# Kernel optimization log

Hardware: AMD Instinct MI355X
Metric: run time of the kernel (lower is better)

The kernel has to match this reference:

```python
import math
import jax, jax.numpy as jnp
import numpy as np

# Dims (match init_kwargs)
B, S, HID = 2, 2048, 2048
H, KVH, D = 16, 8, 128
ATTN_H = 8                      # softmax heads (head_split_dict)
TN_H = H - ATTN_H               # linear (tnorm) heads
N_REP = H // KVH                # GQA repeat factor
FIRST_TOKENS, LAST_TOKENS = 64, 512  # global prefix + band width for custom mask
EPS = 1e-6
ROPE_BASE = 1e6
SCALE = 1.0 / math.sqrt(D)


def _rope_tables(seq_len):
    inv_freq = 1.0 / (ROPE_BASE ** (jnp.arange(0, D, 2, dtype=jnp.float32) / D))
    t = jnp.arange(seq_len, dtype=jnp.float32)
    freqs = jnp.outer(t, inv_freq)                 # [S, D/2]
    emb = jnp.concatenate([freqs, freqs], axis=-1)  # [S, D]
    return jnp.cos(emb), jnp.sin(emb)


def _rotate_half(x):
    x1, x2 = jnp.split(x, 2, axis=-1)
    return jnp.concatenate([-x2, x1], axis=-1)


def _apply_rope(x, cos, sin):
    # x: [B, h, S, D], cos/sin: [S, D]
    return x * cos[None, None] + _rotate_half(x) * sin[None, None]


def _rms_norm(x):
    # SimpleRMSNorm: computed in fp32, no learned weight
    xf = x.astype(jnp.float32)
    out = xf * jax.lax.rsqrt(jnp.mean(xf * xf, axis=-1, keepdims=True) + EPS)
    return out.astype(x.dtype)


def setup_inputs() -> dict:
    key = jax.random.key(0)
    ks = jax.random.split(key, 6)
    sc = 0.02
    perm_np = np.array([3, 7, 0, 12, 9, 15, 1, 5, 2, 4, 6, 8, 10, 11, 13, 14], np.int32)
    inv_np = np.zeros(H, np.int32)
    inv_np[perm_np] = np.arange(H, dtype=np.int32)
    return {
        'hidden_states': jax.random.normal(ks[0], (B, S, HID), jnp.float32),
        'q_w': jax.random.normal(ks[1], (HID, HID), jnp.float32) * sc,
        'q_b': jnp.zeros((HID,), jnp.float32),
        'k_w': jax.random.normal(ks[2], (KVH * D, HID), jnp.float32) * sc,
        'k_b': jnp.zeros((KVH * D,), jnp.float32),
        'v_w': jax.random.normal(ks[3], (KVH * D, HID), jnp.float32) * sc,
        'v_b': jnp.zeros((KVH * D,), jnp.float32),
        'o_w': jax.random.normal(ks[4], (HID, HID), jnp.float32) * sc,
        'head_policy': jnp.array([1, 0, 1, 0, 1, 0, 1, 0], dtype=bool),
        'perm': jnp.asarray(perm_np),
        'inv_perm': jnp.asarray(inv_np),
    }


def _custom_mask(head_policy):
    # create_custom_causal_mask: banded causal + global prefix for heads with
    # policy==False; plain causal for heads with policy==True. Additive mask.
    qi = jnp.arange(S)[:, None]
    ki = jnp.arange(S)[None, :]
    causal = ki <= qi
    band = causal & ((qi - ki) < LAST_TOKENS)
    band = band | ((ki < FIRST_TOKENS) & (qi >= FIRST_TOKENS))
    neg = jnp.finfo(jnp.float32).min
    orig = jnp.where(causal, 0.0, neg)
    new = jnp.where(band, 0.0, neg)
    return jnp.where(head_policy[:, None, None], orig, new), causal  # [ATTN_H,S,S]


def reference(hidden_states, q_w, q_b, k_w, k_b, v_w, v_b, o_w,
              head_policy, perm, inv_perm):
    dt = hidden_states.dtype
    q = hidden_states @ q_w.T + q_b           # [B,S,HID]
    k = hidden_states @ k_w.T + k_b           # [B,S,KVH*D]
    v = hidden_states @ v_w.T + v_b

    # head permutation on q, then split softmax vs tnorm heads
    q = q.reshape(B, S, H, D)[:, :, perm, :]
    q = jnp.transpose(q, (0, 2, 1, 3))        # [B,H,S,D]
    kh = jnp.transpose(k.reshape(B, S, KVH, D), (0, 2, 1, 3))  # [B,KVH,S,D]
    vh = jnp.transpose(v.reshape(B, S, KVH, D), (0, 2, 1, 3))

    cos, sin = _rope_tables(S)
    q = _apply_rope(q, cos, sin)              # rope on all q heads (both branches)
    kh = _apply_rope(kh, cos, sin)

    # repeat_kv (GQA) then head permutation
    k_all = jnp.repeat(kh, N_REP, axis=1)[:, perm]  # [B,H,S,D]
    v_all = jnp.repeat(vh, N_REP, axis=1)[:, perm]

    # ---- softmax branch (first ATTN_H heads), custom banded/global mask ----
    mask, causal = _custom_mask(head_policy)
    logits = jnp.einsum('bhqd,bhkd->bhqk', q[:, :ATTN_H], k_all[:, :ATTN_H]) * SCALE
    logits = logits + mask[None]
    probs = jax.nn.softmax(logits.astype(jnp.float32), axis=-1).astype(dt)
    out_sm = jnp.einsum('bhqk,bhkd->bhqd', probs, v_all[:, :ATTN_H])
    out_sm = jnp.transpose(out_sm, (0, 2, 1, 3)).reshape(B, S, ATTN_H * D)

    # ---- linear (tnorm) branch (remaining heads): masked qk^T @ v + RMSNorm ----
    w = jnp.einsum('bhqd,bhkd->bhqk', q[:, ATTN_H:], k_all[:, ATTN_H:]) * SCALE
    w = jnp.where(causal[None, None], w, jnp.zeros((), dt))
    out_tn = jnp.einsum('bhqk,bhkd->bhqd', w, v_all[:, ATTN_H:])
    out_tn = jnp.transpose(out_tn, (0, 2, 1, 3)).reshape(B, S, TN_H * D)
    out_tn = _rms_norm(out_tn)

    # concat heads, undo permutation, output projection
    out = jnp.concatenate([out_sm, out_tn], axis=-1)
    out = out.reshape(B, S, H, D)[:, :, inv_perm, :].reshape(B, S, HID)
    return out @ o_w.T
```

## Files before the change

kernel.cpp:

```cpp
#include <hip/hip_runtime.h>
#include <hip/hip_bf16.h>
#include <stdint.h>

#define AS1 __attribute__((address_space(1)))
#define AS3 __attribute__((address_space(3)))

typedef __bf16 bf16x8 __attribute__((ext_vector_type(8)));
typedef unsigned short u16x8 __attribute__((ext_vector_type(8)));
typedef float f32x4 __attribute__((ext_vector_type(4)));

static __device__ __forceinline__ unsigned short f2bf(float f) {
  unsigned u = __float_as_uint(f);
  u += 0x7fffu + ((u >> 16) & 1u);
  return (unsigned short)(u >> 16);
}
static __device__ __forceinline__ float bf2f(unsigned short h) {
  return __uint_as_float(((unsigned)h) << 16);
}
static __device__ __forceinline__ bf16x8 ld_frag(const unsigned short* p) {
  union { u16x8 u; bf16x8 b; } c;
  c.u = *(const u16x8*)p;
  return c.b;
}
static __device__ __forceinline__ void gload16(const void* g, void* l) {
  __builtin_amdgcn_global_load_lds((AS1 const void*)g, (AS3 void*)l, 16, 0, 0);
}
#define MFMA(a, b, c) __builtin_amdgcn_mfma_f32_16x16x32_bf16(a, b, c, 0, 0, 0)
#define BAR asm volatile("s_barrier" ::: "memory")
#define VM4 asm volatile("s_waitcnt vmcnt(4)" ::: "memory")

__global__ __launch_bounds__(256)
void cvt_all(const float* __restrict__ hs, const float* __restrict__ qw,
             const float* __restrict__ kw, const float* __restrict__ vw,
             unsigned short* __restrict__ hbf, unsigned short* __restrict__ wqkv) {
  long i = (long)blockIdx.x * 256 + threadIdx.x;
  const float* src; unsigned short* dst; long off;
  if (i < 2097152)      { src = hs; dst = hbf;            off = i; }
  else if (i < 3145728) { src = qw; dst = wqkv;           off = i - 2097152; }
  else if (i < 3670016) { src = kw; dst = wqkv + 4194304; off = i - 3145728; }
  else                  { src = vw; dst = wqkv + 6291456; off = i - 3670016; }
  float4 f = *(const float4*)&src[off * 4];
  ushort4 u;
  u.x = f2bf(f.x); u.y = f2bf(f.y); u.z = f2bf(f.z); u.w = f2bf(f.w);
  *(ushort4*)&dst[off * 4] = u;
}

__global__ __launch_bounds__(256)
void cvt4(const float* __restrict__ in, unsigned short* __restrict__ out, long n) {
  long i = ((long)blockIdx.x * 256 + threadIdx.x) * 4;
  if (i >= n) return;
  float4 f = *(const float4*)&in[i];
  ushort4 u;
  u.x = f2bf(f.x); u.y = f2bf(f.y); u.z = f2bf(f.z); u.w = f2bf(f.w);
  *(ushort4*)&out[i] = u;
}

__global__ __launch_bounds__(256)
void rope_apply(unsigned short* __restrict__ qh, unsigned short* __restrict__ kh) {
  long i = (long)blockIdx.x * 256 + threadIdx.x;
  const long QT = (long)2 * 16 * 2048 * 64;
  unsigned short* p; long rem; float outsc;
  if (i < QT) { p = qh; rem = i; outsc = 0.08838834764831845f; }
  else        { p = kh; rem = i - QT; outsc = 1.0f; }
  int j = (int)(rem & 63);
  long row = rem >> 6;
  int s = (int)(row & 2047);
  unsigned short* x = p + row * 128;
  float inv = exp2f(-0.31143075889569023f * (float)j);
  float f = (float)s * inv;
  float sn, c;
  sincosf(f, &sn, &c);
  float x1 = bf2f(x[j]), x2 = bf2f(x[j + 64]);
  x[j]      = f2bf((x1 * c - x2 * sn) * outsc);
  x[j + 64] = f2bf((x2 * c + x1 * sn) * outsc);
}

__global__ __launch_bounds__(512, 2)
void gemm256_qkv(const unsigned short* __restrict__ A,
                 const unsigned short* __restrict__ Bw,
                 const float* __restrict__ qb, const float* __restrict__ kb,
                 const float* __restrict__ vb,
                 unsigned short* __restrict__ qh, unsigned short* __restrict__ kh,
                 unsigned short* __restrict__ vT) {
  constexpr int K = 2048, NT = K / 64, NIT = NT / 2;
  __shared__ alignas(16) unsigned short LDS[65536];
  const int id = blockIdx.x;
  const int lg = (id & 7) * 32 + (id >> 3);
  const int bm = lg >> 4, bn = lg & 15;
  const int tid = threadIdx.x;
  const int wid = tid >> 6, lane = tid & 63;
  const int wr = wid >> 2, wc = wid & 3;
  const int l15 = lane & 15, lhi = lane >> 4;
  const int rsw = (l15 & 7) << 3;
  const int srow0 = wid * 8 + (lane >> 3);
  const int scol = ((lane & 7) ^ (lane >> 3)) * 8;
  const unsigned short* Ag = A + (long)(bm * 256) * K;
  const unsigned short* Bg = Bw + (long)(bn * 256) * K;
  unsigned short* Al = LDS;
  unsigned short* Bl = LDS + 32768;

#define STG(gb, lb, p, h, t) do {                                              \
    int tc = (t) < NT ? (t) : NT - 1;                                          \
    gload16((gb) + (long)((h) * 128 + srow0) * K + tc * 64 + scol,             \
            (lb) + (p) * 16384 + (h) * 8192 + wid * 512);                      \
    gload16((gb) + (long)((h) * 128 + 64 + srow0) * K + tc * 64 + scol,        \
            (lb) + (p) * 16384 + (h) * 8192 + 4096 + wid * 512);               \
  } while (0)

#define LDA(p, mh) do {                                                        \
    _Pragma("unroll") for (int m4 = 0; m4 < 4; ++m4)                           \
    _Pragma("unroll") for (int kk = 0; kk < 2; ++kk)                           \
      afr[m4][kk] = ld_frag(&Al[(p) * 16384 +                                  \
          (wr * 128 + (mh) * 64 + m4 * 16 + l15) * 64 +                        \
          ((kk * 32 + lhi * 8) ^ rsw)]);                                       \
  } while (0)

#define LDB(p, nh) do {                                                        \
    _Pragma("unroll") for (int n2 = 0; n2 < 2; ++n2)                           \
    _Pragma("unroll") for (int kk = 0; kk < 2; ++kk)                           \
      bfr[nh][n2][kk] = ld_frag(&Bl[(p) * 16384 +                              \
          (wc * 64 + (nh) * 32 + n2 * 16 + l15) * 64 +                         \
          ((kk * 32 + lhi * 8) ^ rsw)]);                                       \
  } while (0)

#define QUAD(mh, nh) do {                                                      \
    __builtin_amdgcn_s_setprio(1);                                             \
    _Pragma("unroll") for (int m4 = 0; m4 < 4; ++m4)                           \
    _Pragma("unroll") for (int n2 = 0; n2 < 2; ++n2)                           \
    _Pragma("unroll") for (int kk = 0; kk < 2; ++kk)                           \
      acc[(mh) * 4 + m4][(nh) * 2 + n2] =                                      \
          MFMA(afr[m4][kk], bfr[nh][n2][kk], acc[(mh) * 4 + m4][(nh) * 2 + n2]);\
    __builtin_amdgcn_s_setprio(0);                                             \
  } while (0)

  f32x4 acc[8][4] = {};
  bf16x8 afr[4][2], bfr[2][2][2];

  STG(Bg, Bl, 0, 0, 0); STG(Bg, Bl, 0, 1, 0);
  STG(Ag, Al, 0, 0, 0); STG(Ag, Al, 0, 1, 0);
  STG(Bg, Bl, 1, 0, 1); STG(Bg, Bl, 1, 1, 1);
  VM4; BAR;

  for (int it = 0; it < NIT; ++it) {
    const int T = 2 * it;
    LDA(0, 0); LDB(0, 0); STG(Ag, Al, 1, 0, T + 1);
    BAR; QUAD(0, 0); BAR;
    LDB(0, 1);            STG(Ag, Al, 1, 1, T + 1);
    BAR; QUAD(0, 1); BAR;
    LDA(0, 1);            STG(Bg, Bl, 0, 0, T + 2);
    BAR; QUAD(1, 0); BAR;
                          STG(Bg, Bl, 0, 1, T + 2);
    VM4; BAR; QUAD(1, 1); BAR;
    LDA(1, 0); LDB(1, 0); STG(Ag, Al, 0, 0, T + 2);
    BAR; QUAD(0, 0); BAR;
    LDB(1, 1);            STG(Ag, Al, 0, 1, T + 2);
    BAR; QUAD(0, 1); BAR;
    LDA(1, 1);            STG(Bg, Bl, 1, 0, T + 3);
    BAR; QUAD(1, 0); BAR;
                          STG(Bg, Bl, 1, 1, T + 3);
    VM4; BAR; QUAD(1, 1); BAR;
  }

  const int r0 = bm * 256 + wr * 128, c0 = bn * 256 + wc * 64;
#pragma unroll
  for (int m = 0; m < 8; ++m) {
#pragma unroll
    for (int n = 0; n < 4; ++n) {
#pragma unroll
      for (int j = 0; j < 4; ++j) {
        int row = r0 + m * 16 + lhi * 4 + j;
        int col = c0 + n * 16 + l15;
        float v = acc[m][n][j];
        int b = row >> 11, s = row & 2047;
        if (col < 2048) {
          v += qb[col];
          qh[((long)(b * 16 + (col >> 7)) * 2048 + s) * 128 + (col & 127)] = f2bf(v);
        } else if (col < 3072) {
          int c = col - 2048; v += kb[c];
          kh[((long)(b * 8 + (c >> 7)) * 2048 + s) * 128 + (c & 127)] = f2bf(v);
        } else {
          int c = col - 3072; v += vb[c];
          vT[((long)(b * 8 + (c >> 7)) * 128 + (c & 127)) * 2048 + s] = f2bf(v);
        }
      }
    }
  }
#undef STG
#undef LDA
#undef LDB
#undef QUAD
}

__global__ __launch_bounds__(256, 2)
void gemm_bt(const unsigned short* __restrict__ A,
             const unsigned short* __restrict__ Bw,
             int K, int N, float* __restrict__ Cout) {
  __shared__ alignas(16) unsigned short As[128 * 64];
  __shared__ alignas(16) unsigned short Bs[128 * 64];
  const int bm = blockIdx.x, bn = blockIdx.y;
  const int tid = threadIdx.x;
  const int w = tid >> 6, l = tid & 63;
  const int wm = w >> 1, wn = w & 1;
  const int l15 = l & 15, lhi = l >> 4;
  f32x4 acc[4][4] = {};
  const unsigned short* aptr = A + ((long)(bm * 128 + w * 8 + (l >> 3))) * K + (l & 7) * 8;
  const unsigned short* bptr = Bw + ((long)(bn * 128 + w * 8 + (l >> 3))) * K + (l & 7) * 8;
  unsigned short* asb = &As[w * 8 * 64];
  unsigned short* bsb = &Bs[w * 8 * 64];
  for (int k0 = 0; k0 < K; k0 += 64) {
#pragma unroll
    for (int i = 0; i < 4; ++i) {
      gload16(aptr + (long)i * 32 * K, asb + i * 2048);
      gload16(bptr + (long)i * 32 * K, bsb + i * 2048);
    }
    aptr += 64; bptr += 64;
    __syncthreads();
#pragma unroll
    for (int kk = 0; kk < 2; ++kk) {
      bf16x8 af[4], bfr[4];
#pragma unroll
      for (int m = 0; m < 4; ++m)
        af[m] = ld_frag(&As[(wm * 64 + m * 16 + l15) * 64 + kk * 32 + lhi * 8]);
#pragma unroll
      for (int n = 0; n < 4; ++n)
        bfr[n] = ld_frag(&Bs[(wn * 64 + n * 16 + l15) * 64 + kk * 32 + lhi * 8]);
#pragma unroll
      for (int m = 0; m < 4; ++m)
#pragma unroll
        for (int n = 0; n < 4; ++n)
          acc[m][n] = MFMA(af[m], bfr[n], acc[m][n]);
    }
    __syncthreads();
  }
#pragma unroll
  for (int m = 0; m < 4; ++m)
#pragma unroll
    for (int n = 0; n < 4; ++n)
#pragma unroll
      for (int j = 0; j < 4; ++j) {
        int row = bm * 128 + wm * 64 + m * 16 + lhi * 4 + j;
        int col = bn * 128 + wn * 64 + n * 16 + l15;
        Cout[(long)row * N + col] = acc[m][n][j];
      }
}

__global__ __launch_bounds__(256, 4)
void attn_all(const unsigned short* __restrict__ qheads,
              const unsigned short* __restrict__ kheads,
              const unsigned short* __restrict__ vT,
              unsigned short* __restrict__ aout,
              unsigned short* __restrict__ tnb,
              unsigned short* __restrict__ pao0, unsigned short* __restrict__ pao1,
              float* __restrict__ pl0, float* __restrict__ pl1,
              const int* __restrict__ perm) {
  __shared__ alignas(16) unsigned short Ks[64 * 128];
  __shared__ alignas(16) unsigned short Vs[128 * 64];
  __shared__ alignas(16) unsigned short Ps[4][16 * 64];
  const int bx = 47 - blockIdx.x;
  const int hy = blockIdx.y;
  const int b = blockIdx.z;
  const bool sm = hy < 8;
  const bool banded = sm && ((hy & 1) != 0);
  int t, kst, ket;
  bool partial = false, slice1 = false;
  if (banded) {
    if (bx >= 32) return;
    t = bx; kst = 0; ket = t;
  } else if (bx < 16) {
    t = bx; kst = 0; ket = t;
  } else if (bx < 32) {
    t = bx; int h = (t + 2) >> 1; kst = 0; ket = h - 1; partial = true;
  } else {
    t = bx - 16; int h = (t + 2) >> 1; kst = h; ket = t; partial = true; slice1 = true;
  }
  const int q0 = t * 64;
  const int qhd = perm[hy];
  const int kvh = qhd >> 1;
  const int tid = threadIdx.x, w = tid >> 6, l = tid & 63, l15 = l & 15, lhi = l >> 4;
  const unsigned short* Qg = qheads + ((long)(b * 16 + qhd) * 2048 + q0) * 128;
  const unsigned short* Kg = kheads + (long)(b * 8 + kvh) * 2048 * 128;
  const unsigned short* Vg = vT + (long)(b * 8 + kvh) * 128 * 2048;
  bf16x8 qf[4];
#pragma unroll
  for (int c = 0; c < 4; ++c)
    qf[c] = ld_frag(Qg + (w * 16 + l15) * 128 + c * 32 + lhi * 8);
  f32x4 ao[8] = {};
  float lsum[4] = {0.f, 0.f, 0.f, 0.f};
  const int krow = w * 4 + (l >> 4);
  const long kgoff = (long)krow * 128 + (((l & 15) * 8) ^ ((krow & 7) << 3));
  unsigned short* kdst = &Ks[w * 512];
  const int vrow = w * 8 + (l >> 3);
  const long vgoff = (long)vrow * 2048 + (((l & 7) * 8) ^ ((vrow & 7) << 3));
  unsigned short* vdst = &Vs[w * 512];
  const int rsw15 = (l15 & 7) << 3;

  for (int k0 = kst * 64; k0 <= ket * 64; k0 += 64) {
    if (banded && k0 >= 64 && q0 - k0 >= 575) continue;
    __syncthreads();
#pragma unroll
    for (int p = 0; p < 4; ++p)
      gload16(Kg + (long)(k0 + p * 16) * 128 + kgoff, kdst + p * 2048);
#pragma unroll
    for (int p = 0; p < 4; ++p)
      gload16(Vg + (long)p * 32 * 2048 + k0 + vgoff, vdst + p * 2048);
    __syncthreads();
    f32x4 sacc[4] = {};
    __builtin_amdgcn_s_setprio(1);
#pragma unroll
    for (int c = 0; c < 4; ++c) {
#pragma unroll
      for (int ks = 0; ks < 4; ++ks) {
        bf16x8 kf = ld_frag(&Ks[(ks * 16 + l15) * 128 + ((c * 32 + lhi * 8) ^ rsw15)]);
        sacc[ks] = MFMA(qf[c], kf, sacc[ks]);
      }
    }
    __builtin_amdgcn_s_setprio(0);
    const int qrb = q0 + w * 16 + lhi * 4;
#pragma unroll
    for (int j = 0; j < 4; ++j) {
      const int q = qrb + j;
      const int prow = lhi * 4 + j;
      const int psw = (prow & 7) << 3;
#pragma unroll
      for (int ks = 0; ks < 4; ++ks) {
        int k = k0 + ks * 16 + l15;
        bool ok = (k <= q) && (!banded || k < 64 || (q - k) < 512);
        float p;
        if (sm) { p = ok ? __expf(sacc[ks][j]) : 0.f; lsum[j] += p; }
        else    { p = ok ? sacc[ks][j] : 0.f; }
        Ps[w][prow * 64 + ((ks * 16 + l15) ^ psw)] = f2bf(p);
      }
    }
    bf16x8 pa0 = ld_frag(&Ps[w][l15 * 64 + ((lhi * 8) ^ rsw15)]);
    bf16x8 pa1 = ld_frag(&Ps[w][l15 * 64 + ((32 + lhi * 8) ^ rsw15)]);
    __builtin_amdgcn_s_setprio(1);
#pragma unroll
    for (int n = 0; n < 8; ++n) {
      bf16x8 vf0 = ld_frag(&Vs[(n * 16 + l15) * 64 + ((lhi * 8) ^ rsw15)]);
      bf16x8 vf1 = ld_frag(&Vs[(n * 16 + l15) * 64 + ((32 + lhi * 8) ^ rsw15)]);
      ao[n] = MFMA(pa0, vf0, ao[n]);
      ao[n] = MFMA(pa1, vf1, ao[n]);
    }
    __builtin_amdgcn_s_setprio(0);
  }

  if (partial) {
    const int hc = sm ? (hy >> 1) : (hy - 4);
    const long rbase = (long)(b * 12 + hc) * 1024 + (q0 - 1024);
    unsigned short* pb = (slice1 ? pao1 : pao0) + rbase * 128;
    float* plb = (slice1 ? pl1 : pl0) + rbase;
#pragma unroll
    for (int j = 0; j < 4; ++j) {
      const int r = w * 16 + lhi * 4 + j;
      if (sm) {
        float s = lsum[j];
#pragma unroll
        for (int d = 1; d < 16; d <<= 1) s += __shfl_xor(s, d);
        if (l15 == 0) plb[r] = s;
      }
#pragma unroll
      for (int n = 0; n < 8; ++n)
        pb[(long)r * 128 + n * 16 + l15] = f2bf(ao[n][j]);
    }
  } else if (sm) {
#pragma unroll
    for (int j = 0; j < 4; ++j) {
      float s = lsum[j];
#pragma unroll
      for (int d = 1; d < 16; d <<= 1) s += __shfl_xor(s, d);
      float inv = 1.0f / s;
      int q = q0 + w * 16 + lhi * 4 + j;
      unsigned short* o = aout + ((long)b * 2048 + q) * 2048 + qhd * 128;
#pragma unroll
      for (int n = 0; n < 8; ++n) o[n * 16 + l15] = f2bf(ao[n][j] * inv);
    }
  } else {
    const int hidx = hy - 8;
#pragma unroll
    for (int j = 0; j < 4; ++j) {
      int q = q0 + w * 16 + lhi * 4 + j;
      unsigned short* o = tnb + ((long)b * 2048 + q) * 1024 + hidx * 128;
#pragma unroll
      for (int n = 0; n < 8; ++n) o[n * 16 + l15] = f2bf(ao[n][j]);
    }
  }
}

__global__ __launch_bounds__(256)
void combine(const unsigned short* __restrict__ pao0,
             const unsigned short* __restrict__ pao1,
             const float* __restrict__ pl0, const float* __restrict__ pl1,
             unsigned short* __restrict__ aout, unsigned short* __restrict__ tnb,
             const int* __restrict__ perm) {
  long i = (long)blockIdx.x * 256 + threadIdx.x;
  long row = i >> 7;
  int col = (int)(i & 127);
  int b = (int)(row / 12288);
  int rem = (int)(row - (long)b * 12288);
  int hc = rem >> 10;
  int q = 1024 + (rem & 1023);
  float a = bf2f(pao0[i]) + bf2f(pao1[i]);
  if (hc < 4) {
    int qhd = perm[hc * 2];
    float lv = pl0[row] + pl1[row];
    aout[((long)b * 2048 + q) * 2048 + qhd * 128 + col] = f2bf(a / lv);
  } else {
    tnb[((long)b * 2048 + q) * 1024 + (hc - 4) * 128 + col] = f2bf(a);
  }
}

__global__ __launch_bounds__(256)
void rms_scatter(const unsigned short* __restrict__ tnb,
                 unsigned short* __restrict__ aout,
                 const int* __restrict__ perm) {
  __shared__ float wsum[4];
  int row = blockIdx.x, tid = threadIdx.x;
  const unsigned short* x = tnb + (long)row * 1024;
  ushort4 u = *(const ushort4*)&x[tid * 4];
  float v0 = bf2f(u.x), v1 = bf2f(u.y), v2 = bf2f(u.z), v3 = bf2f(u.w);
  float ss = v0 * v0 + v1 * v1 + v2 * v2 + v3 * v3;
#pragma unroll
  for (int d = 1; d < 64; d <<= 1) ss += __shfl_xor(ss, d);
  if ((tid & 63) == 0) wsum[tid >> 6] = ss;
  __syncthreads();
  float tot = wsum[0] + wsum[1] + wsum[2] + wsum[3];
  float r = rsqrtf(tot * (1.0f / 1024.0f) + 1e-6f);
  int slot = perm[8 + (tid >> 5)];
  unsigned short* o = aout + (long)row * 2048 + slot * 128 + ((tid * 4) & 127);
  o[0] = f2bf(v0 * r); o[1] = f2bf(v1 * r); o[2] = f2bf(v2 * r); o[3] = f2bf(v3 * r);
}

extern "C" void kernel_launch(void* const* d_in, const int* in_sizes, int n_in,
                              void* d_out, int out_size, void* d_ws, size_t ws_size,
                              hipStream_t stream) {
  const float* hs  = (const float*)d_in[0];
  const float* q_w = (const float*)d_in[1];
  const float* q_b = (const float*)d_in[2];
  const float* k_w = (const float*)d_in[3];
  const float* k_b = (const float*)d_in[4];
  const float* v_w = (const float*)d_in[5];
  const float* v_b = (const float*)d_in[6];
  const float* o_w = (const float*)d_in[7];
  const int* perm  = (const int*)d_in[9];

  char* ws = (char*)d_ws;
  unsigned short* hbf  = (unsigned short*)(ws + 0);
  unsigned short* wqkv = (unsigned short*)(ws + 16777216);
  unsigned short* kh   = (unsigned short*)(ws + 33554432);
  unsigned short* vT   = (unsigned short*)(ws + 41943040);
  char* dob = (char*)d_out;
  unsigned short* qh   = (unsigned short*)dob;
  unsigned short* pao0 = (unsigned short*)(dob + 16777216);
  unsigned short* pao1 = (unsigned short*)(dob + 23068672);
  float* pl0           = (float*)(dob + 29360128);
  float* pl1           = (float*)(dob + 29458432);
  unsigned short* aout = hbf;
  unsigned short* tnb  = wqkv;
  unsigned short* owb  = kh;
  float* outF = (float*)d_out;

  cvt_all<<<16384, 256, 0, stream>>>(hs, q_w, k_w, v_w, hbf, wqkv);
  gemm256_qkv<<<256, 512, 0, stream>>>(hbf, wqkv, q_b, k_b, v_b, qh, kh, vT);
  rope_apply<<<24576, 256, 0, stream>>>(qh, kh);
  attn_all<<<dim3(48, 16, 2), 256, 0, stream>>>(qh, kh, vT, aout, tnb,
                                                pao0, pao1, pl0, pl1, perm);
  combine<<<12288, 256, 0, stream>>>(pao0, pao1, pl0, pl1, aout, tnb, perm);
  cvt4<<<4096, 256, 0, stream>>>(o_w, owb, 4194304);
  rms_scatter<<<4096, 256, 0, stream>>>(tnb, aout, perm);
  gemm_bt<<<dim3(32, 16), 256, 0, stream>>>(aout, owb, 2048, 2048, outF);
}
```

Baseline: 276.5 us.

## Split PV matmul across warps by output columns instead of query rows

The P·V step now shares the probability tiles of all four warps through LDS. Each warp computes 32 of the 128 output columns for all 64 query rows, rather than all columns for its own 16 rows. This cuts the V-fragment LDS reads per warp from 16 to 4, and the extra work is reading the other warps' P tiles. It adds a block-wide barrier per key tile and an LDS buffer for the row sums, and the epilogue changes to match the new ownership of the output.

```diff
diff --git a/kernel.cpp b/kernel.cpp
--- a/kernel.cpp
+++ b/kernel.cpp
@@ -256,6 +256,7 @@
   __shared__ alignas(16) unsigned short Ks[64 * 128];
   __shared__ alignas(16) unsigned short Vs[128 * 64];
   __shared__ alignas(16) unsigned short Ps[4][16 * 64];
+  __shared__ float Ls[64];
   const int bx = 47 - blockIdx.x;
   const int hy = blockIdx.y;
   const int b = blockIdx.z;
@@ -284,7 +285,7 @@
 #pragma unroll
   for (int c = 0; c < 4; ++c)
     qf[c] = ld_frag(Qg + (w * 16 + l15) * 128 + c * 32 + lhi * 8);
-  f32x4 ao[8] = {};
+  f32x4 ao[2][4] = {};
   float lsum[4] = {0.f, 0.f, 0.f, 0.f};
   const int krow = w * 4 + (l >> 4);
   const long kgoff = (long)krow * 128 + (((l & 15) * 8) ^ ((krow & 7) << 3));
@@ -331,58 +332,72 @@
         Ps[w][prow * 64 + ((ks * 16 + l15) ^ psw)] = f2bf(p);
       }
     }
-    bf16x8 pa0 = ld_frag(&Ps[w][l15 * 64 + ((lhi * 8) ^ rsw15)]);
-    bf16x8 pa1 = ld_frag(&Ps[w][l15 * 64 + ((32 + lhi * 8) ^ rsw15)]);
+    __syncthreads();
     __builtin_amdgcn_s_setprio(1);
-#pragma unroll
-    for (int n = 0; n < 8; ++n) {
-      bf16x8 vf0 = ld_frag(&Vs[(n * 16 + l15) * 64 + ((lhi * 8) ^ rsw15)]);
-      bf16x8 vf1 = ld_frag(&Vs[(n * 16 + l15) * 64 + ((32 + lhi * 8) ^ rsw15)]);
-      ao[n] = MFMA(pa0, vf0, ao[n]);
-      ao[n] = MFMA(pa1, vf1, ao[n]);
+    bf16x8 vf0a = ld_frag(&Vs[((w * 2) * 16 + l15) * 64 + ((lhi * 8) ^ rsw15)]);
+    bf16x8 vf1a = ld_frag(&Vs[((w * 2) * 16 + l15) * 64 + ((32 + lhi * 8) ^ rsw15)]);
+    bf16x8 vf0b = ld_frag(&Vs[((w * 2 + 1) * 16 + l15) * 64 + ((lhi * 8) ^ rsw15)]);
+    bf16x8 vf1b = ld_frag(&Vs[((w * 2 + 1) * 16 + l15) * 64 + ((32 + lhi * 8) ^ rsw15)]);
+#pragma unroll
+    for (int wc = 0; wc < 4; ++wc) {
+      bf16x8 pa0 = ld_frag(&Ps[wc][l15 * 64 + ((lhi * 8) ^ rsw15)]);
+      bf16x8 pa1 = ld_frag(&Ps[wc][l15 * 64 + ((32 + lhi * 8) ^ rsw15)]);
+      ao[0][wc] = MFMA(pa0, vf0a, ao[0][wc]);
+      ao[0][wc] = MFMA(pa1, vf1a, ao[0][wc]);
+      ao[1][wc] = MFMA(pa0, vf0b, ao[1][wc]);
+      ao[1][wc] = MFMA(pa1, vf1b, ao[1][wc]);
     }
     __builtin_amdgcn_s_setprio(0);
   }
+
+#pragma unroll
+  for (int j = 0; j < 4; ++j) {
+    float s = lsum[j];
+#pragma unroll
+    for (int d = 1; d < 16; d <<= 1) s += __shfl_xor(s, d);
+    if (l15 == 0) Ls[w * 16 + lhi * 4 + j] = s;
+  }
+  __syncthreads();
 
   if (partial) {
     const int hc = sm ? (hy >> 1) : (hy - 4);
     const long rbase = (long)(b * 12 + hc) * 1024 + (q0 - 1024);
     unsigned short* pb = (slice1 ? pao1 : pao0) + rbase * 128;
     float* plb = (slice1 ? pl1 : pl0) + rbase;
-#pragma unroll
-    for (int j = 0; j < 4; ++j) {
-      const int r = w * 16 + lhi * 4 + j;
-      if (sm) {
-        float s = lsum[j];
-#pragma unroll
-        for (int d = 1; d < 16; d <<= 1) s += __shfl_xor(s, d);
-        if (l15 == 0) plb[r] = s;
-      }
-#pragma unroll
-      for (int n = 0; n < 8; ++n)
-        pb[(long)r * 128 + n * 16 + l15] = f2bf(ao[n][j]);
-    }
+    if (sm && tid < 64) plb[tid] = Ls[tid];
+#pragma unroll
+    for (int wc = 0; wc < 4; ++wc)
+#pragma unroll
+      for (int j = 0; j < 4; ++j) {
+        int r = wc * 16 + lhi * 4 + j;
+#pragma unroll
+        for (int n2 = 0; n2 < 2; ++n2)
+          pb[(long)r * 128 + (w * 2 + n2) * 16 + l15] = f2bf(ao[n2][wc][j]);
+      }
   } else if (sm) {
 #pragma unroll
-    for (int j = 0; j < 4; ++j) {
-      float s = lsum[j];
-#pragma unroll
-      for (int d = 1; d < 16; d <<= 1) s += __shfl_xor(s, d);
-      float inv = 1.0f / s;
-      int q = q0 + w * 16 + lhi * 4 + j;
-      unsigned short* o = aout + ((long)b * 2048 + q) * 2048 + qhd * 128;
-#pragma unroll
-      for (int n = 0; n < 8; ++n) o[n * 16 + l15] = f2bf(ao[n][j] * inv);
-    }
+    for (int wc = 0; wc < 4; ++wc)
+#pragma unroll
+      for (int j = 0; j < 4; ++j) {
+        int r = wc * 16 + lhi * 4 + j;
+        float inv = 1.0f / Ls[r];
+        unsigned short* o = aout + ((long)b * 2048 + q0 + r) * 2048 + qhd * 128;
+#pragma unroll
+        for (int n2 = 0; n2 < 2; ++n2)
+          o[(w * 2 + n2) * 16 + l15] = f2bf(ao[n2][wc][j] * inv);
+      }
   } else {
     const int hidx = hy - 8;
 #pragma unroll
-    for (int j = 0; j < 4; ++j) {
-      int q = q0 + w * 16 + lhi * 4 + j;
-      unsigned short* o = tnb + ((long)b * 2048 + q) * 1024 + hidx * 128;
-#pragma unroll
-      for (int n = 0; n < 8; ++n) o[n * 16 + l15] = f2bf(ao[n][j]);
-    }
+    for (int wc = 0; wc < 4; ++wc)
+#pragma unroll
+      for (int j = 0; j < 4; ++j) {
+        int q = q0 + wc * 16 + lhi * 4 + j;
+        unsigned short* o = tnb + ((long)b * 2048 + q) * 1024 + hidx * 128;
+#pragma unroll
+        for (int n2 = 0; n2 < 2; ++n2)
+          o[(w * 2 + n2) * 16 + l15] = f2bf(ao[n2][wc][j]);
+      }
   }
 }
 
```

Result: no change. 274.2 us (-0.8%).
